# Kernel tuning notes

Measured on AMD Instinct MI355X. Metric: run time of the kernel, lower is better.

Reference implementation:

```python
import jax, jax.numpy as jnp
import numpy as np

B, S, D, H, DK = 8, 1024, 1024, 16, 64
DV = D // H  # 64


def setup_inputs() -> dict:
    key = jax.random.key(0)
    ks = jax.random.split(key, 9)
    s = 1.0 / np.sqrt(D)
    return {
        "x": jax.random.normal(ks[0], (B, S, D), dtype=jnp.float32),
        "masks": jnp.ones((B, S), dtype=jnp.int32),
        "Wq": jax.random.normal(ks[1], (D, H * DK), dtype=jnp.float32) * s,
        "bq": jnp.zeros((H * DK,), dtype=jnp.float32),
        "Wk": jax.random.normal(ks[2], (D, H * DK), dtype=jnp.float32) * s,
        "bk": jnp.zeros((H * DK,), dtype=jnp.float32),
        "Wv": jax.random.normal(ks[3], (D, H * DV), dtype=jnp.float32) * s,
        "bv": jnp.zeros((H * DV,), dtype=jnp.float32),
        "Wo": jax.random.normal(ks[4], (H * DV, D), dtype=jnp.float32) * s,
        "bo": jnpp_zeros() if False else jnp.zeros((D,), dtype=jnp.float32),
    }


def reference(x, masks, Wq, bq, Wk, bk, Wv, bv, Wo, bo):
    # projections -> [B, H, S, d]
    q = (x @ Wq + bq).reshape(B, S, H, DK).transpose(0, 2, 1, 3)
    k = (x @ Wk + bk).reshape(B, S, H, DK).transpose(0, 2, 1, 3)
    v = (x @ Wv + bv).reshape(B, S, H, DV).transpose(0, 2, 1, 3)
    # scaled dot-product attention with padding mask
    logits = jnp.einsum('bhqd,bhkd->bhqk', q, k) / jnp.sqrt(jnp.float32(DK))
    mask = masks[:, None, None, :]  # [B,1,1,S]
    logits = jnp.where(mask == 0, jnp.float32(-1e9), logits)
    scores = jax.nn.softmax(logits, axis=-1)
    out = jnp.einsum('bhqk,bhkd->bhqd', scores, v)
    out = out.transpose(0, 2, 1, 3).reshape(B, S, H * DV)
    # output projection; dropout is identity in eval mode
    return out @ Wo + bo
```

## Files before the change

kernel.cpp:

```cpp
#include <hip/hip_runtime.h>
#include <stdint.h>

#define B_ 8
#define S_ 1024
#define D_ 1024
#define H_ 16
#define DK_ 64
#define DV_ 64

typedef __attribute__((ext_vector_type(8))) short short8;
typedef __attribute__((ext_vector_type(4))) float f32x4;

__device__ __forceinline__ unsigned short f2bf(float f) {
  union { float f; unsigned u; } v; v.f = f;
  return (unsigned short)((v.u + 0x7fffu + ((v.u >> 16) & 1u)) >> 16);
}
__device__ __forceinline__ unsigned short f2bf_trunc(float f) {
  union { float f; unsigned u; } v; v.f = f;
  return (unsigned short)(v.u >> 16);
}

__device__ __forceinline__ void ld_lds16(const unsigned short* g, unsigned short* l) {
  __builtin_amdgcn_global_load_lds((const __attribute__((address_space(1))) void*)g,
                                   (__attribute__((address_space(3))) void*)l, 16, 0, 0);
}

__global__ __launch_bounds__(256) void prep_kernel(const float* __restrict__ x,
                                                   unsigned short* __restrict__ xb,
                                                   const float* __restrict__ W0,
                                                   const float* __restrict__ W1,
                                                   const float* __restrict__ W2,
                                                   const float* __restrict__ W3,
                                                   unsigned short* __restrict__ T0,
                                                   unsigned short* __restrict__ T1,
                                                   unsigned short* __restrict__ T2,
                                                   unsigned short* __restrict__ T3) {
  const int z = blockIdx.z;
  if (z >= 4) {
    size_t blk = (size_t)(z - 4) * 256 + blockIdx.y * 16 + blockIdx.x;
    size_t i = (blk * 256 + threadIdx.x) * 4;
    float4 v = *(const float4*)(x + i);
    ushort4 o;
    o.x = f2bf(v.x); o.y = f2bf(v.y); o.z = f2bf(v.z); o.w = f2bf(v.w);
    *(ushort4*)(xb + i) = o;
    return;
  }
  __shared__ __align__(16) unsigned short tl[64][65];
  const float* W; unsigned short* Wt;
  switch (z) {
    case 0: W = W0; Wt = T0; break;
    case 1: W = W1; Wt = T1; break;
    case 2: W = W2; Wt = T2; break;
    default: W = W3; Wt = T3; break;
  }
  const int xx = threadIdx.x & 63;
  const int y4 = threadIdx.x >> 6;
  const int bn = blockIdx.x * 64;
  const int bk = blockIdx.y * 64;
  #pragma unroll
  for (int r = y4; r < 64; r += 4)
    tl[r][xx] = f2bf(W[(size_t)(bk + r) * 1024 + bn + xx]);
  __syncthreads();
  #pragma unroll
  for (int r = y4; r < 64; r += 4)
    Wt[(size_t)(bn + r) * 1024 + bk + xx] = tl[xx][r];
}

__device__ __forceinline__ void stage_tile64(const unsigned short* __restrict__ G,
                                             unsigned short* __restrict__ Ls,
                                             int t, int wslot, size_t rowstride, int k0) {
  #pragma unroll
  for (int i = 0; i < 4; i++) {
    int s = i * 256 + t;
    int r = s >> 3, c = (s & 7) ^ (r & 7);
    ld_lds16(G + (size_t)r * rowstride + k0 + c * 8, &Ls[(i * 256 + wslot) * 8]);
  }
}

__global__ __launch_bounds__(256) void gemm_qkv(const unsigned short* __restrict__ A,
                                                const unsigned short* __restrict__ Bt,
                                                const float* __restrict__ bq,
                                                const float* __restrict__ bk,
                                                const float* __restrict__ bv,
                                                const int* __restrict__ masks,
                                                unsigned short* __restrict__ q,
                                                unsigned short* __restrict__ kk,
                                                unsigned short* __restrict__ vT) {
  const int K = 1024;
  __shared__ __align__(16) unsigned short As[128 * 64];
  __shared__ __align__(16) unsigned short Bs[128 * 64];
  const int t = threadIdx.x;
  const int wave = t >> 6, lane = t & 63;
  const int l15 = lane & 15, quad = lane >> 4;
  const int l7 = l15 & 7;
  const int bm = blockIdx.y * 128, bn = blockIdx.x * 128;
  const int wm = (wave & 1) * 64, wn = (wave >> 1) * 64;
  const bool vsec = (blockIdx.x >= 16);
  const int wslot = (t & ~63);

  f32x4 acc[4][4] = {};
  const unsigned short* Ag = A + (size_t)bm * K;
  const unsigned short* Bg = Bt + (size_t)bn * K;

  for (int k0 = 0; k0 < K; k0 += 64) {
    __syncthreads();
    stage_tile64(Ag, As, t, wslot, K, k0);
    stage_tile64(Bg, Bs, t, wslot, K, k0);
    __syncthreads();
    #pragma unroll
    for (int kf = 0; kf < 2; kf++) {
      short8 af[4], bf[4];
      #pragma unroll
      for (int mi = 0; mi < 4; mi++)
        af[mi] = *(const short8*)&As[(wm + mi * 16 + l15) * 64 + (((kf << 2) | quad) ^ l7) * 8];
      #pragma unroll
      for (int ni = 0; ni < 4; ni++)
        bf[ni] = *(const short8*)&Bs[(wn + ni * 16 + l15) * 64 + (((kf << 2) | quad) ^ l7) * 8];
      if (vsec) {
        #pragma unroll
        for (int mi = 0; mi < 4; mi++)
          #pragma unroll
          for (int ni = 0; ni < 4; ni++)
            acc[mi][ni] = __builtin_amdgcn_mfma_f32_16x16x32_bf16(bf[ni], af[mi], acc[mi][ni], 0, 0, 0);
      } else {
        #pragma unroll
        for (int mi = 0; mi < 4; mi++)
          #pragma unroll
          for (int ni = 0; ni < 4; ni++)
            acc[mi][ni] = __builtin_amdgcn_mfma_f32_16x16x32_bf16(af[mi], bf[ni], acc[mi][ni], 0, 0, 0);
      }
    }
  }

  if (!vsec) {
    int sec = blockIdx.x >> 3;
    const float* bsel = (sec == 0) ? bq : bk;
    unsigned short* dst = (sec == 0) ? q : kk;
    float scale = (sec == 0) ? 0.180336880f : 1.0f;
    #pragma unroll
    for (int ni = 0; ni < 4; ni++) {
      int c = ((bn & 1023) + wn + ni * 16 + l15);
      float bvv = bsel[c];
      int hh = c >> 6, d = c & 63;
      #pragma unroll
      for (int mi = 0; mi < 4; mi++) {
        int row0 = bm + wm + mi * 16 + quad * 4;
        #pragma unroll
        for (int r = 0; r < 4; r++) {
          int row = row0 + r;
          int b = row >> 10, s = row & 1023;
          dst[(((size_t)(b * H_ + hh)) * S_ + s) * DK_ + d] = f2bf((acc[mi][ni][r] + bvv) * scale);
        }
      }
    }
  } else {
    #pragma unroll
    for (int ni = 0; ni < 4; ni++) {
      int cbase = (bn & 1023) + wn + ni * 16;
      #pragma unroll
      for (int mi = 0; mi < 4; mi++) {
        int row = bm + wm + mi * 16 + l15;
        int b = row >> 10, s = row & 1023;
        float mf = (masks[b * S_ + s] != 0) ? 1.0f : 0.0f;
        #pragma unroll
        for (int r = 0; r < 4; r++) {
          int c = cbase + quad * 4 + r;
          int hh = c >> 6, d = c & 63;
          vT[(((size_t)(b * H_ + hh)) * DV_ + d) * S_ + s] = f2bf((acc[mi][ni][r] + bv[c]) * mf);
        }
      }
    }
  }
}

__global__ __launch_bounds__(256) void gemm_out(const unsigned short* __restrict__ A,
                                                const unsigned short* __restrict__ Bt,
                                                const float* __restrict__ bias,
                                                float* __restrict__ Cout) {
  const int K = 1024, N = 1024;
  __shared__ __align__(16) unsigned short As[128 * 64];
  __shared__ __align__(16) unsigned short Bs[128 * 64];
  const int t = threadIdx.x;
  const int wave = t >> 6, lane = t & 63;
  const int l15 = lane & 15, quad = lane >> 4;
  const int l7 = l15 & 7;
  const int bm = blockIdx.y * 128, bn = blockIdx.x * 128;
  const int wm = (wave & 1) * 64, wn = (wave >> 1) * 64;
  const int wslot = (t & ~63);

  f32x4 acc[4][4] = {};
  const unsigned short* Ag = A + (size_t)bm * K;
  const unsigned short* Bg = Bt + (size_t)bn * K;

  for (int k0 = 0; k0 < K; k0 += 64) {
    __syncthreads();
    stage_tile64(Ag, As, t, wslot, K, k0);
    stage_tile64(Bg, Bs, t, wslot, K, k0);
    __syncthreads();
    #pragma unroll
    for (int kf = 0; kf < 2; kf++) {
      short8 af[4], bf[4];
      #pragma unroll
      for (int mi = 0; mi < 4; mi++)
        af[mi] = *(const short8*)&As[(wm + mi * 16 + l15) * 64 + (((kf << 2) | quad) ^ l7) * 8];
      #pragma unroll
      for (int ni = 0; ni < 4; ni++)
        bf[ni] = *(const short8*)&Bs[(wn + ni * 16 + l15) * 64 + (((kf << 2) | quad) ^ l7) * 8];
      #pragma unroll
      for (int mi = 0; mi < 4; mi++)
        #pragma unroll
        for (int ni = 0; ni < 4; ni++)
          acc[mi][ni] = __builtin_amdgcn_mfma_f32_16x16x32_bf16(af[mi], bf[ni], acc[mi][ni], 0, 0, 0);
    }
  }

  #pragma unroll
  for (int ni = 0; ni < 4; ni++) {
    int col = bn + wn + ni * 16 + l15;
    float bvv = bias[col];
    #pragma unroll
    for (int mi = 0; mi < 4; mi++) {
      int row0 = bm + wm + mi * 16 + quad * 4;
      #pragma unroll
      for (int r = 0; r < 4; r++)
        Cout[(size_t)(row0 + r) * N + col] = acc[mi][ni][r] + bvv;
    }
  }
}

#define PLD 72
#define VROWS 65
__global__ __launch_bounds__(256) void attn_kernel(const unsigned short* __restrict__ Q,
                                                   const unsigned short* __restrict__ Kb,
                                                   const unsigned short* __restrict__ Vt,
                                                   const int* __restrict__ masks,
                                                   unsigned short* __restrict__ O) {
  __shared__ __align__(16) unsigned short Pl[128 * PLD];
  __shared__ __align__(16) unsigned short Ks[2 * 64 * 64];
  __shared__ __align__(16) unsigned short Vs[(2 * VROWS + 15) * 64];
  const int t = threadIdx.x;
  const int wave = t >> 6, lane = t & 63;
  const int l15 = lane & 15, quad = lane >> 4;
  const int l7 = l15 & 7;
  const int bh = blockIdx.x;
  const int qt = blockIdx.y;
  const int b = bh >> 4, h = bh & 15;

  const unsigned short* Qg = Q + ((size_t)bh * S_ + qt * 128) * DK_;
  const unsigned short* Kg = Kb + (size_t)bh * S_ * DK_;
  const unsigned short* Vg = Vt + (size_t)bh * DV_ * S_;
  const int wslot = (t & ~63);

  int mv[4];
  #pragma unroll
  for (int j = 0; j < 4; j++)
    mv[j] = masks[b * S_ + (j * 4 + wave) * 64 + lane];

  short8 aq[2][2];
  #pragma unroll
  for (int mb = 0; mb < 2; mb++)
    #pragma unroll
    for (int kf = 0; kf < 2; kf++)
      aq[mb][kf] = *(const short8*)(Qg + (size_t)(wave * 32 + mb * 16 + l15) * 64 + kf * 32 + quad * 8);

  auto stage = [&](int kt, int buf) {
    const unsigned short* Kt = Kg + (size_t)kt * 64 * DK_;
    unsigned short* Kd = &Ks[buf * 4096];
    unsigned short* Vd = &Vs[buf * (VROWS * 64)];
    #pragma unroll
    for (int i = 0; i < 2; i++) {
      int p = i * 256 + t;
      int rk = p >> 3, ck = (p & 7) ^ (rk & 7);
      ld_lds16(Kt + (size_t)rk * DK_ + ck * 8, &Kd[(i * 256 + wslot) * 8]);
      ld_lds16(Vg + (size_t)rk * S_ + kt * 64 + ck * 8, &Vd[(i * 256 + wslot) * 8]);
    }
    if (wave == (kt & 3))
      Vd[64 * 64 + lane] = (mv[kt >> 2] != 0) ? (unsigned short)0x3F80 : (unsigned short)0;
  };

  f32x4 o_acc[2][5] = {};

  stage(0, 0);
  __syncthreads();

  #pragma unroll 2
  for (int kt = 0; kt < 16; kt++) {
    const int cur = kt & 1;
    if (kt < 15) stage(kt + 1, cur ^ 1);
    const unsigned short* Kc = &Ks[cur * 4096];
    const unsigned short* Vc = &Vs[cur * (VROWS * 64)];

    f32x4 sc[2][4];
    #pragma unroll
    for (int n = 0; n < 4; n++) {
      short8 bk0 = *(const short8*)&Kc[(n * 16 + l15) * 64 + (quad ^ l7) * 8];
      short8 bk1 = *(const short8*)&Kc[(n * 16 + l15) * 64 + ((4 + quad) ^ l7) * 8];
      #pragma unroll
      for (int mb = 0; mb < 2; mb++) {
        f32x4 c = {};
        c = __builtin_amdgcn_mfma_f32_16x16x32_bf16(bk0, aq[mb][0], c, 0, 0, 0);
        c = __builtin_amdgcn_mfma_f32_16x16x32_bf16(bk1, aq[mb][1], c, 0, 0, 0);
        sc[mb][n] = c;
      }
    }
    #pragma unroll
    for (int mb = 0; mb < 2; mb++)
      #pragma unroll
      for (int n = 0; n < 4; n++) {
        ushort4 pk;
        pk.x = f2bf_trunc(__builtin_amdgcn_exp2f(sc[mb][n][0]));
        pk.y = f2bf_trunc(__builtin_amdgcn_exp2f(sc[mb][n][1]));
        pk.z = f2bf_trunc(__builtin_amdgcn_exp2f(sc[mb][n][2]));
        pk.w = f2bf_trunc(__builtin_amdgcn_exp2f(sc[mb][n][3]));
        *(ushort4*)&Pl[(wave * 32 + mb * 16 + l15) * PLD + n * 16 + quad * 4] = pk;
      }
    #pragma unroll
    for (int kf = 0; kf < 2; kf++) {
      short8 ap[2];
      #pragma unroll
      for (int mb = 0; mb < 2; mb++)
        ap[mb] = *(const short8*)&Pl[(wave * 32 + mb * 16 + l15) * PLD + kf * 32 + quad * 8];
      #pragma unroll
      for (int n = 0; n < 5; n++) {
        short8 bv = *(const short8*)&Vc[(n * 16 + l15) * 64 + ((kf * 4 + quad) ^ l7) * 8];
        #pragma unroll
        for (int mb = 0; mb < 2; mb++)
          o_acc[mb][n] = __builtin_amdgcn_mfma_f32_16x16x32_bf16(ap[mb], bv, o_acc[mb][n], 0, 0, 0);
      }
    }
    __syncthreads();
  }

  #pragma unroll
  for (int mb = 0; mb < 2; mb++)
    #pragma unroll
    for (int r = 0; r < 4; r++) {
      float l = __shfl(o_acc[mb][4][r], lane & 48, 64);
      float inv = __builtin_amdgcn_rcpf(l);
      int qrow = qt * 128 + wave * 32 + mb * 16 + quad * 4 + r;
      #pragma unroll
      for (int n = 0; n < 4; n++) {
        int col = h * 64 + n * 16 + l15;
        O[((size_t)b * S_ + qrow) * D_ + col] = f2bf(o_acc[mb][n][r] * inv);
      }
    }
}

extern "C" void kernel_launch(void* const* d_in, const int* in_sizes, int n_in,
                              void* d_out, int out_size, void* d_ws, size_t ws_size,
                              hipStream_t stream) {
  (void)in_sizes; (void)n_in; (void)out_size; (void)ws_size;
  const float* x  = (const float*)d_in[0];
  const int* masks = (const int*)d_in[1];
  const float* Wq = (const float*)d_in[2];
  const float* bq = (const float*)d_in[3];
  const float* Wk = (const float*)d_in[4];
  const float* bk = (const float*)d_in[5];
  const float* Wv = (const float*)d_in[6];
  const float* bv = (const float*)d_in[7];
  const float* Wo = (const float*)d_in[8];
  const float* bo = (const float*)d_in[9];

  char* p = (char*)d_ws;
  unsigned short* xb    = (unsigned short*)p; p += (size_t)8192 * 1024 * 2;
  unsigned short* WqkvT = (unsigned short*)p; p += (size_t)3072 * 1024 * 2;
  unsigned short* WoT   = (unsigned short*)p; p += (size_t)1024 * 1024 * 2;
  unsigned short* q     = (unsigned short*)p; p += (size_t)8192 * 1024 * 2;
  unsigned short* kk    = (unsigned short*)p; p += (size_t)8192 * 1024 * 2;
  unsigned short* vT    = (unsigned short*)p; p += (size_t)8192 * 1024 * 2;
  unsigned short* at    = (unsigned short*)p; p += (size_t)8192 * 1024 * 2;

  prep_kernel<<<dim3(16, 16, 36), 256, 0, stream>>>(
      x, xb, Wq, Wk, Wv, Wo,
      WqkvT, WqkvT + (size_t)1024 * 1024, WqkvT + (size_t)2048 * 1024, WoT);
  gemm_qkv<<<dim3(24, 64), 256, 0, stream>>>(xb, WqkvT, bq, bk, bv, masks, q, kk, vT);
  attn_kernel<<<dim3(128, 8), 256, 0, stream>>>(q, kk, vT, masks, at);
  gemm_out<<<dim3(8, 64), 256, 0, stream>>>(at, WoT, bo, (float*)d_out);
}
```

Before: 241.4 us.

## Rewrite QKV and output GEMMs as 8-wave double-buffered pipelined kernels

```diff
diff --git a/kernel.cpp b/kernel.cpp
--- a/kernel.cpp
+++ b/kernel.cpp
@@ -66,71 +66,162 @@
     Wt[(size_t)(bn + r) * 1024 + bk + xx] = tl[xx][r];
 }
 
-__device__ __forceinline__ void stage_tile64(const unsigned short* __restrict__ G,
-                                             unsigned short* __restrict__ Ls,
-                                             int t, int wslot, size_t rowstride, int k0) {
-  #pragma unroll
-  for (int i = 0; i < 4; i++) {
-    int s = i * 256 + t;
-    int r = s >> 3, c = (s & 7) ^ (r & 7);
-    ld_lds16(G + (size_t)r * rowstride + k0 + c * 8, &Ls[(i * 256 + wslot) * 8]);
-  }
-}
-
-__global__ __launch_bounds__(256) void gemm_qkv(const unsigned short* __restrict__ A,
-                                                const unsigned short* __restrict__ Bt,
-                                                const float* __restrict__ bq,
-                                                const float* __restrict__ bk,
-                                                const float* __restrict__ bv,
-                                                const int* __restrict__ masks,
-                                                unsigned short* __restrict__ q,
-                                                unsigned short* __restrict__ kk,
-                                                unsigned short* __restrict__ vT) {
-  const int K = 1024;
-  __shared__ __align__(16) unsigned short As[128 * 64];
-  __shared__ __align__(16) unsigned short Bs[128 * 64];
+
+struct SJob { const unsigned short* g; unsigned short* l; };
+
+__device__ __forceinline__ void stage128(const unsigned short* __restrict__ G,
+                                         unsigned short* __restrict__ L, int t) {
+  #pragma unroll
+  for (int i = 0; i < 2; i++) {
+    int s = i * 512 + t;
+    int r = s >> 3, cb = s & 7;
+    int c = cb ^ (r & 7);
+    ld_lds16(G + (size_t)r * 1024 + c * 8, L + (size_t)s * 8);
+  }
+}
+
+template <bool SW>
+__device__ __forceinline__ f32x4 MM(short8 a, short8 b, f32x4 c) {
+  if constexpr (SW) return __builtin_amdgcn_mfma_f32_16x16x32_bf16(b, a, c, 0, 0, 0);
+  else              return __builtin_amdgcn_mfma_f32_16x16x32_bf16(a, b, c, 0, 0, 0);
+}
+
+template <bool SW, int VM>
+__device__ __forceinline__ void ktile(const unsigned short* __restrict__ As_,
+                                      const unsigned short* __restrict__ Bs_,
+                                      f32x4 (&acc)[4][4],
+                                      SJob s0, SJob s1, SJob s2,
+                                      int t, int wm, int wn, int l15, int quad, int l7) {
+  const int cb0 = (quad ^ l7) * 8;
+  const int cb1 = ((4 | quad) ^ l7) * 8;
+  short8 b0[4], b1[4];
+
+  short8 a0k0 = *(const short8*)&As_[(wm + 0 * 16 + l15) * 64 + cb0];
+  short8 a1k0 = *(const short8*)&As_[(wm + 1 * 16 + l15) * 64 + cb0];
+  #pragma unroll
+  for (int ni = 0; ni < 4; ni++)
+    b0[ni] = *(const short8*)&Bs_[(wn + ni * 16 + l15) * 64 + cb0];
+  if (s0.g) stage128(s0.g, s0.l, t);
+  __builtin_amdgcn_s_barrier();
+  asm volatile("s_waitcnt lgkmcnt(0)" ::: "memory");
+  __builtin_amdgcn_s_setprio(1);
+  #pragma unroll
+  for (int ni = 0; ni < 4; ni++) {
+    acc[0][ni] = MM<SW>(a0k0, b0[ni], acc[0][ni]);
+    acc[1][ni] = MM<SW>(a1k0, b0[ni], acc[1][ni]);
+  }
+  __builtin_amdgcn_s_setprio(0);
+  __builtin_amdgcn_s_barrier();
+
+  short8 a0k1 = *(const short8*)&As_[(wm + 0 * 16 + l15) * 64 + cb1];
+  short8 a1k1 = *(const short8*)&As_[(wm + 1 * 16 + l15) * 64 + cb1];
+  #pragma unroll
+  for (int ni = 0; ni < 4; ni++)
+    b1[ni] = *(const short8*)&Bs_[(wn + ni * 16 + l15) * 64 + cb1];
+  if (s1.g) stage128(s1.g, s1.l, t);
+  __builtin_amdgcn_s_barrier();
+  asm volatile("s_waitcnt lgkmcnt(0)" ::: "memory");
+  __builtin_amdgcn_s_setprio(1);
+  #pragma unroll
+  for (int ni = 0; ni < 4; ni++) {
+    acc[0][ni] = MM<SW>(a0k1, b1[ni], acc[0][ni]);
+    acc[1][ni] = MM<SW>(a1k1, b1[ni], acc[1][ni]);
+  }
+  __builtin_amdgcn_s_setprio(0);
+  __builtin_amdgcn_s_barrier();
+
+  short8 a2k0 = *(const short8*)&As_[(wm + 2 * 16 + l15) * 64 + cb0];
+  short8 a3k0 = *(const short8*)&As_[(wm + 3 * 16 + l15) * 64 + cb0];
+  if (s2.g) stage128(s2.g, s2.l, t);
+  __builtin_amdgcn_s_barrier();
+  asm volatile("s_waitcnt lgkmcnt(0)" ::: "memory");
+  __builtin_amdgcn_s_setprio(1);
+  #pragma unroll
+  for (int ni = 0; ni < 4; ni++) {
+    acc[2][ni] = MM<SW>(a2k0, b0[ni], acc[2][ni]);
+    acc[3][ni] = MM<SW>(a3k0, b0[ni], acc[3][ni]);
+  }
+  __builtin_amdgcn_s_setprio(0);
+  __builtin_amdgcn_s_barrier();
+
+  short8 a2k1 = *(const short8*)&As_[(wm + 2 * 16 + l15) * 64 + cb1];
+  short8 a3k1 = *(const short8*)&As_[(wm + 3 * 16 + l15) * 64 + cb1];
+  __builtin_amdgcn_s_barrier();
+  asm volatile("s_waitcnt lgkmcnt(0)" ::: "memory");
+  __builtin_amdgcn_s_setprio(1);
+  #pragma unroll
+  for (int ni = 0; ni < 4; ni++) {
+    acc[2][ni] = MM<SW>(a2k1, b1[ni], acc[2][ni]);
+    acc[3][ni] = MM<SW>(a3k1, b1[ni], acc[3][ni]);
+  }
+  __builtin_amdgcn_s_setprio(0);
+  if constexpr (VM == 2) asm volatile("s_waitcnt vmcnt(2)" ::: "memory");
+  else                   asm volatile("s_waitcnt vmcnt(0)" ::: "memory");
+  __builtin_amdgcn_s_barrier();
+}
+
+template <bool SW>
+__device__ __forceinline__ void gemm_core(const unsigned short* __restrict__ Ag,
+                                          const unsigned short* __restrict__ Bg,
+                                          unsigned short* __restrict__ Asl,
+                                          unsigned short* __restrict__ Bsl,
+                                          f32x4 (&acc)[4][4],
+                                          int t, int wm, int wn, int l15, int quad, int l7) {
+  stage128(Ag, &Asl[0], t);
+  stage128(Ag + 128 * 1024, &Asl[8192], t);
+  stage128(Bg, &Bsl[0], t);
+  stage128(Bg + 64, &Bsl[8192], t);
+  asm volatile("s_waitcnt vmcnt(2)" ::: "memory");
+  __builtin_amdgcn_s_barrier();
+
+  #pragma unroll 1
+  for (int tt = 0; tt < 7; tt++) {
+    const int J0 = 2 * tt;
+    ktile<SW, 2>(&Asl[0], &Bsl[0], acc,
+                 SJob{Ag + (size_t)(J0 + 1) * 64,              &Asl[16384]},
+                 SJob{Ag + (size_t)(J0 + 1) * 64 + 128 * 1024, &Asl[16384 + 8192]},
+                 SJob{Bg + (size_t)(J0 + 2) * 64,              &Bsl[0]},
+                 t, wm, wn, l15, quad, l7);
+    ktile<SW, 2>(&Asl[16384], &Bsl[8192], acc,
+                 SJob{Ag + (size_t)(J0 + 2) * 64,              &Asl[0]},
+                 SJob{Ag + (size_t)(J0 + 2) * 64 + 128 * 1024, &Asl[8192]},
+                 SJob{Bg + (size_t)(J0 + 3) * 64,              &Bsl[8192]},
+                 t, wm, wn, l15, quad, l7);
+  }
+  ktile<SW, 0>(&Asl[0], &Bsl[0], acc,
+               SJob{Ag + (size_t)15 * 64,              &Asl[16384]},
+               SJob{Ag + (size_t)15 * 64 + 128 * 1024, &Asl[16384 + 8192]},
+               SJob{nullptr, nullptr},
+               t, wm, wn, l15, quad, l7);
+  ktile<SW, 0>(&Asl[16384], &Bsl[8192], acc,
+               SJob{nullptr, nullptr}, SJob{nullptr, nullptr}, SJob{nullptr, nullptr},
+               t, wm, wn, l15, quad, l7);
+}
+
+__global__ __launch_bounds__(512, 2) void gemm_qkv8(const unsigned short* __restrict__ A,
+                                                    const unsigned short* __restrict__ Bt,
+                                                    const float* __restrict__ bq,
+                                                    const float* __restrict__ bk,
+                                                    const float* __restrict__ bv,
+                                                    const int* __restrict__ masks,
+                                                    unsigned short* __restrict__ q,
+                                                    unsigned short* __restrict__ kk,
+                                                    unsigned short* __restrict__ vT) {
+  extern __shared__ unsigned short lds[];
+  unsigned short* Asl = lds;
+  unsigned short* Bsl = lds + 2 * 16384;
   const int t = threadIdx.x;
-  const int wave = t >> 6, lane = t & 63;
-  const int l15 = lane & 15, quad = lane >> 4;
-  const int l7 = l15 & 7;
-  const int bm = blockIdx.y * 128, bn = blockIdx.x * 128;
-  const int wm = (wave & 1) * 64, wn = (wave >> 1) * 64;
+  const int w = t >> 6, lane = t & 63;
+  const int l15 = lane & 15, quad = lane >> 4, l7 = l15 & 7;
+  const int bm = blockIdx.y * 256, bn = blockIdx.x * 128;
+  const int wm = (w >> 1) * 64, wn = (w & 1) * 64;
   const bool vsec = (blockIdx.x >= 16);
-  const int wslot = (t & ~63);
+  const unsigned short* Ag = A + (size_t)bm * 1024;
+  const unsigned short* Bg = Bt + (size_t)bn * 1024;
 
   f32x4 acc[4][4] = {};
-  const unsigned short* Ag = A + (size_t)bm * K;
-  const unsigned short* Bg = Bt + (size_t)bn * K;
-
-  for (int k0 = 0; k0 < K; k0 += 64) {
-    __syncthreads();
-    stage_tile64(Ag, As, t, wslot, K, k0);
-    stage_tile64(Bg, Bs, t, wslot, K, k0);
-    __syncthreads();
-    #pragma unroll
-    for (int kf = 0; kf < 2; kf++) {
-      short8 af[4], bf[4];
-      #pragma unroll
-      for (int mi = 0; mi < 4; mi++)
-        af[mi] = *(const short8*)&As[(wm + mi * 16 + l15) * 64 + (((kf << 2) | quad) ^ l7) * 8];
-      #pragma unroll
-      for (int ni = 0; ni < 4; ni++)
-        bf[ni] = *(const short8*)&Bs[(wn + ni * 16 + l15) * 64 + (((kf << 2) | quad) ^ l7) * 8];
-      if (vsec) {
-        #pragma unroll
-        for (int mi = 0; mi < 4; mi++)
-          #pragma unroll
-          for (int ni = 0; ni < 4; ni++)
-            acc[mi][ni] = __builtin_amdgcn_mfma_f32_16x16x32_bf16(bf[ni], af[mi], acc[mi][ni], 0, 0, 0);
-      } else {
-        #pragma unroll
-        for (int mi = 0; mi < 4; mi++)
-          #pragma unroll
-          for (int ni = 0; ni < 4; ni++)
-            acc[mi][ni] = __builtin_amdgcn_mfma_f32_16x16x32_bf16(af[mi], bf[ni], acc[mi][ni], 0, 0, 0);
-      }
-    }
-  }
+  if (!vsec) gemm_core<false>(Ag, Bg, Asl, Bsl, acc, t, wm, wn, l15, quad, l7);
+  else       gemm_core<true >(Ag, Bg, Asl, Bsl, acc, t, wm, wn, l15, quad, l7);
 
   if (!vsec) {
     int sec = blockIdx.x >> 3;
@@ -139,7 +230,7 @@
     float scale = (sec == 0) ? 0.180336880f : 1.0f;
     #pragma unroll
     for (int ni = 0; ni < 4; ni++) {
-      int c = ((bn & 1023) + wn + ni * 16 + l15);
+      int c = (bn & 1023) + wn + ni * 16 + l15;
       float bvv = bsel[c];
       int hh = c >> 6, d = c & 63;
       #pragma unroll
@@ -173,46 +264,23 @@
   }
 }
 
-__global__ __launch_bounds__(256) void gemm_out(const unsigned short* __restrict__ A,
-                                                const unsigned short* __restrict__ Bt,
-                                                const float* __restrict__ bias,
-                                                float* __restrict__ Cout) {
-  const int K = 1024, N = 1024;
-  __shared__ __align__(16) unsigned short As[128 * 64];
-  __shared__ __align__(16) unsigned short Bs[128 * 64];
+__global__ __launch_bounds__(512, 2) void gemm_out8(const unsigned short* __restrict__ A,
+                                                    const unsigned short* __restrict__ Bt,
+                                                    const float* __restrict__ bias,
+                                                    float* __restrict__ Cout) {
+  extern __shared__ unsigned short lds[];
+  unsigned short* Asl = lds;
+  unsigned short* Bsl = lds + 2 * 16384;
   const int t = threadIdx.x;
-  const int wave = t >> 6, lane = t & 63;
-  const int l15 = lane & 15, quad = lane >> 4;
-  const int l7 = l15 & 7;
-  const int bm = blockIdx.y * 128, bn = blockIdx.x * 128;
-  const int wm = (wave & 1) * 64, wn = (wave >> 1) * 64;
-  const int wslot = (t & ~63);
+  const int w = t >> 6, lane = t & 63;
+  const int l15 = lane & 15, quad = lane >> 4, l7 = l15 & 7;
+  const int bm = blockIdx.y * 256, bn = blockIdx.x * 128;
+  const int wm = (w >> 1) * 64, wn = (w & 1) * 64;
+  const unsigned short* Ag = A + (size_t)bm * 1024;
+  const unsigned short* Bg = Bt + (size_t)bn * 1024;
 
   f32x4 acc[4][4] = {};
-  const unsigned short* Ag = A + (size_t)bm * K;
-  const unsigned short* Bg = Bt + (size_t)bn * K;
-
-  for (int k0 = 0; k0 < K; k0 += 64) {
-    __syncthreads();
-    stage_tile64(Ag, As, t, wslot, K, k0);
-    stage_tile64(Bg, Bs, t, wslot, K, k0);
-    __syncthreads();
-    #pragma unroll
-    for (int kf = 0; kf < 2; kf++) {
-      short8 af[4], bf[4];
-      #pragma unroll
-      for (int mi = 0; mi < 4; mi++)
-        af[mi] = *(const short8*)&As[(wm + mi * 16 + l15) * 64 + (((kf << 2) | quad) ^ l7) * 8];
-      #pragma unroll
-      for (int ni = 0; ni < 4; ni++)
-        bf[ni] = *(const short8*)&Bs[(wn + ni * 16 + l15) * 64 + (((kf << 2) | quad) ^ l7) * 8];
-      #pragma unroll
-      for (int mi = 0; mi < 4; mi++)
-        #pragma unroll
-        for (int ni = 0; ni < 4; ni++)
-          acc[mi][ni] = __builtin_amdgcn_mfma_f32_16x16x32_bf16(af[mi], bf[ni], acc[mi][ni], 0, 0, 0);
-    }
-  }
+  gemm_core<false>(Ag, Bg, Asl, Bsl, acc, t, wm, wn, l15, quad, l7);
 
   #pragma unroll
   for (int ni = 0; ni < 4; ni++) {
@@ -223,7 +291,7 @@
       int row0 = bm + wm + mi * 16 + quad * 4;
       #pragma unroll
       for (int r = 0; r < 4; r++)
-        Cout[(size_t)(row0 + r) * N + col] = acc[mi][ni][r] + bvv;
+        Cout[(size_t)(row0 + r) * 1024 + col] = acc[mi][ni][r] + bvv;
     }
   }
 }
@@ -370,10 +438,17 @@
   unsigned short* vT    = (unsigned short*)p; p += (size_t)8192 * 1024 * 2;
   unsigned short* at    = (unsigned short*)p; p += (size_t)8192 * 1024 * 2;
 
+  static bool attr_done = false;
+  if (!attr_done) {
+    hipFuncSetAttribute((const void*)gemm_qkv8, hipFuncAttributeMaxDynamicSharedMemorySize, 98304);
+    hipFuncSetAttribute((const void*)gemm_out8, hipFuncAttributeMaxDynamicSharedMemorySize, 98304);
+    attr_done = true;
+  }
+
   prep_kernel<<<dim3(16, 16, 36), 256, 0, stream>>>(
       x, xb, Wq, Wk, Wv, Wo,
       WqkvT, WqkvT + (size_t)1024 * 1024, WqkvT + (size_t)2048 * 1024, WoT);
-  gemm_qkv<<<dim3(24, 64), 256, 0, stream>>>(xb, WqkvT, bq, bk, bv, masks, q, kk, vT);
+  gemm_qkv8<<<dim3(24, 32), 512, 98304, stream>>>(xb, WqkvT, bq, bk, bv, masks, q, kk, vT);
   attn_kernel<<<dim3(128, 8), 256, 0, stream>>>(q, kk, vT, masks, at);
-  gemm_out<<<dim3(8, 64), 256, 0, stream>>>(at, WoT, bo, (float*)d_out);
-}
+  gemm_out8<<<dim3(8, 32), 512, 98304, stream>>>(at, WoT, bo, (float*)d_out);
+}
```

New measurement: 239.3 us. About the same (-0.9%).
